# Kernel tuning notes

Measured on AMD Instinct MI355X. Metric: run time of the kernel, lower is better.

Reference implementation:

```python
import jax, jax.numpy as jnp
import numpy as np

B, T, D = 4, 2048, 768
H = 12
HD = D // H
WINDOW = 128

def setup_inputs() -> dict:
    key = jax.random.key(0)
    k1, k2, k3 = jax.random.split(key, 3)
    x = jax.random.normal(k1, (B, T, D), dtype=jnp.float32)
    Wqkv = jax.random.normal(k2, (D, 3 * D), dtype=jnp.float32) * 0.02
    Wout = jax.random.normal(k3, (D, D), dtype=jnp.float32) * 0.02
    return {"x": x, "Wqkv": Wqkv, "Wout": Wout}

def reference(x, Wqkv, Wout):
    Bx, Tx, Dx = x.shape
    qkv = x @ Wqkv                      # [B,T,3D]
    q, k, v = jnp.split(qkv, 3, axis=-1)
    def heads(t):
        return t.reshape(Bx, Tx, H, HD).transpose(0, 2, 1, 3)  # [B,H,T,hd]
    q, k, v = heads(q), heads(k), heads(v)
    scale = 1.0 / jnp.sqrt(jnp.float32(HD))
    scores = jnp.einsum('bhqd,bhkd->bhqk', q, k) * scale       # [B,H,T,T]
    pos = jnp.arange(Tx)
    dist = pos[None, :] - pos[:, None]                          # j - i
    blocked = (dist > 0) | (dist < -WINDOW)                     # causal band
    scores = jnp.where(blocked[None, None], -jnp.inf, scores)
    attn = jax.nn.softmax(scores, axis=-1)
    out = jnp.einsum('bhqk,bhkd->bhqd', attn, v)                # [B,H,T,hd]
    out = out.transpose(0, 2, 1, 3).reshape(Bx, Tx, Dx)
    return out @ Wout
```

## Files before the change

kernel.cpp:

```cpp
#include <hip/hip_runtime.h>
#include <hip/hip_bf16.h>
#include <stdint.h>

typedef unsigned short u16;
typedef __attribute__((ext_vector_type(8))) short short8;
typedef __attribute__((ext_vector_type(8))) __bf16 bf16x8;
typedef __attribute__((ext_vector_type(4))) float f32x4;

constexpr int Bc  = 4;
constexpr int Tc  = 2048;
constexpr int Dc  = 768;
constexpr int Hc  = 12;
constexpr int WINc = 128;

static __device__ __forceinline__ u16 f2bf(float f) {
  union { float f; uint32_t u; } v; v.f = f;
  uint32_t u = v.u;
  return (u16)((u + 0x7fffu + ((u >> 16) & 1u)) >> 16);
}

static __device__ __forceinline__ f32x4 mfma16x16x32(bf16x8 a, bf16x8 b, f32x4 c) {
  return __builtin_amdgcn_mfma_f32_16x16x32_bf16(a, b, c, 0, 0, 0);
}

#define GLOAD_LDS16(gsrc, ldst)                                                \
  __builtin_amdgcn_global_load_lds(                                            \
      (const __attribute__((address_space(1))) void*)(gsrc),                   \
      (__attribute__((address_space(3))) void*)(ldst), 16, 0, 0)

__global__ __launch_bounds__(256) void prep(const float* __restrict__ x,
                                            u16* __restrict__ xb,
                                            const float* __restrict__ Wqkv,
                                            u16* __restrict__ wqkvT,
                                            const float* __restrict__ Wout,
                                            u16* __restrict__ woutT) {
  __shared__ float tile[64][65];
  const int t = threadIdx.x;
  const int b = blockIdx.x;
  if (b < 6144) {
    const int i = b * 256 + t;
    const float4 f = ((const float4*)x)[i];
    union { u16 h[4]; uint2 u; } pk;
    pk.h[0] = f2bf(f.x); pk.h[1] = f2bf(f.y); pk.h[2] = f2bf(f.z); pk.h[3] = f2bf(f.w);
    ((uint2*)xb)[i] = pk.u;
    return;
  }
  const float* W; u16* WT; int C, bx, by;
  if (b < 6576) { W = Wqkv; WT = wqkvT; C = 2304; const int bb = b - 6144; bx = bb % 36; by = bb / 36; }
  else          { W = Wout; WT = woutT; C = 768;  const int bb = b - 6576; bx = bb % 12; by = bb / 12; }
  const int R = 768;
  const int c0 = bx * 64, r0 = by * 64;
#pragma unroll
  for (int i = 0; i < 16; ++i) {
    const int e = i * 256 + t;
    const int r = e >> 6, c = e & 63;
    tile[r][c] = W[(size_t)(r0 + r) * C + c0 + c];
  }
  __syncthreads();
#pragma unroll
  for (int i = 0; i < 16; ++i) {
    const int e = i * 256 + t;
    const int r = e >> 6, c = e & 63;
    WT[(size_t)(c0 + r) * R + r0 + c] = f2bf(tile[c][r]);
  }
}

template <int EPI>
__global__ __launch_bounds__(256) void gemm_bt(const u16* __restrict__ A,
                                               const u16* __restrict__ Bt,
                                               u16* __restrict__ q_ws,
                                               u16* __restrict__ k_ws,
                                               u16* __restrict__ v_ws,
                                               float* __restrict__ fout) {
  __shared__ u16 As[128][64];
  __shared__ u16 Bs[128][64];
  const int t  = threadIdx.x;
  const int w  = t >> 6, l = t & 63;
  const int lr = l & 15, lh = l >> 4;
  const int wm = w >> 1, wn = w & 1;
  const int m0 = blockIdx.y * 128, n0 = blockIdx.x * 128;

  f32x4 acc[4][4];
#pragma unroll
  for (int mi = 0; mi < 4; ++mi)
#pragma unroll
    for (int ni = 0; ni < 4; ++ni) acc[mi][ni] = f32x4{0.f, 0.f, 0.f, 0.f};

  const int srow = w * 8 + (l >> 3);
  const int scol = ((l & 7) ^ (l >> 3)) * 8;
  const u16* aP = A  + (size_t)(m0 + srow) * 768 + scol;
  const u16* bP = Bt + (size_t)(n0 + srow) * 768 + scol;
  char* asB = (char*)As + w * 1024;
  char* bsB = (char*)Bs + w * 1024;

  for (int kt = 0; kt < 12; ++kt) {
    const int ko = kt * 64;
    __syncthreads();
#pragma unroll
    for (int j = 0; j < 4; ++j) {
      GLOAD_LDS16(aP + ko + j * (32 * 768), asB + j * 4096);
      GLOAD_LDS16(bP + ko + j * (32 * 768), bsB + j * 4096);
    }
    __syncthreads();

#pragma unroll
    for (int kk = 0; kk < 2; ++kk) {
      const int cb = (kk * 64 + lh * 16) ^ ((lr & 7) << 4);
      bf16x8 af[4], bfr[4];
#pragma unroll
      for (int mi = 0; mi < 4; ++mi)
        af[mi] = *(const bf16x8*)((const char*)As + (wm * 64 + mi * 16 + lr) * 128 + cb);
#pragma unroll
      for (int ni = 0; ni < 4; ++ni)
        bfr[ni] = *(const bf16x8*)((const char*)Bs + (wn * 64 + ni * 16 + lr) * 128 + cb);
#pragma unroll
      for (int mi = 0; mi < 4; ++mi)
#pragma unroll
        for (int ni = 0; ni < 4; ++ni)
          acc[mi][ni] = mfma16x16x32(af[mi], bfr[ni], acc[mi][ni]);
    }
  }

  if (EPI == 0) {
#pragma unroll
    for (int mi = 0; mi < 4; ++mi)
#pragma unroll
      for (int ni = 0; ni < 4; ++ni) {
        const int col   = n0 + wn * 64 + ni * 16 + lr;
        const int which = col / 768;
        const int rem   = col - which * 768;
        const int h     = rem >> 6, d = rem & 63;
        u16* dst = (which == 0) ? q_ws : ((which == 1) ? k_ws : v_ws);
        const float scl = (which == 0) ? 0.125f : 1.0f;
#pragma unroll
        for (int r = 0; r < 4; ++r) {
          const int m  = m0 + wm * 64 + mi * 16 + lh * 4 + r;
          const int bb = m >> 11, tt = m & 2047;
          dst[(((size_t)(bb * Hc + h) * Tc + tt) << 6) + d] = f2bf(acc[mi][ni][r] * scl);
        }
      }
  } else {
#pragma unroll
    for (int mi = 0; mi < 4; ++mi)
#pragma unroll
      for (int ni = 0; ni < 4; ++ni) {
        const int col = n0 + wn * 64 + ni * 16 + lr;
#pragma unroll
        for (int r = 0; r < 4; ++r) {
          const int m = m0 + wm * 64 + mi * 16 + lh * 4 + r;
          fout[(size_t)m * 768 + col] = acc[mi][ni][r];
        }
      }
  }
}

__global__ __launch_bounds__(256) void swa_attn(const u16* __restrict__ Q,
                                                const u16* __restrict__ Kk,
                                                const u16* __restrict__ V,
                                                u16* __restrict__ Out) {
  __shared__ u16 Ks[3][64][72];
  __shared__ u16 Vt[3][64][72];
  __shared__ u16 Ps[4][16][72];

  const int t  = threadIdx.x;
  const int w  = t >> 6, l = t & 63;
  const int lr = l & 15, lh = l >> 4;
  const int bh = blockIdx.y;
  const int q0 = blockIdx.x * 64;
  const size_t hb = (size_t)bh * Tc * 64;

  const int kb_lo = (q0 >= WINc) ? q0 - WINc : 0;
  const int nt    = ((q0 - kb_lo) >> 6) + 1;

  const u16* qrow = Q + hb + (size_t)(q0 + w * 16 + lr) * 64;
  const bf16x8 qa0 = *(const bf16x8*)(qrow + lh * 8);
  const bf16x8 qa1 = *(const bf16x8*)(qrow + 32 + lh * 8);

  const int row = t >> 2, c = (t & 3) * 16;
  short8 kreg[3][2], vreg[3][2];
#pragma unroll
  for (int ti = 0; ti < 3; ++ti) {
    if (ti < nt) {
      const int kb = kb_lo + ti * 64;
      const short8* ksrc = (const short8*)(Kk + hb + (size_t)(kb + row) * 64 + c);
      const short8* vsrc = (const short8*)(V  + hb + (size_t)(kb + row) * 64 + c);
      kreg[ti][0] = ksrc[0]; kreg[ti][1] = ksrc[1];
      vreg[ti][0] = vsrc[0]; vreg[ti][1] = vsrc[1];
    }
  }
#pragma unroll
  for (int ti = 0; ti < 3; ++ti) {
    if (ti < nt) {
      *(short8*)&Ks[ti][row][c]     = kreg[ti][0];
      *(short8*)&Ks[ti][row][c + 8] = kreg[ti][1];
#pragma unroll
      for (int j = 0; j < 8; ++j) {
        Vt[ti][c + j][row]     = (u16)vreg[ti][0][j];
        Vt[ti][c + 8 + j][row] = (u16)vreg[ti][1][j];
      }
    }
  }
  __syncthreads();

  const short8 ones_i = {(short)0x3F80, (short)0x3F80, (short)0x3F80, (short)0x3F80,
                         (short)0x3F80, (short)0x3F80, (short)0x3F80, (short)0x3F80};
  const bf16x8 onesv = *(const bf16x8*)&ones_i;

  float m_r[4];
  f32x4 lacc = f32x4{0.f, 0.f, 0.f, 0.f};
  f32x4 Oa[4];
#pragma unroll
  for (int r = 0; r < 4; ++r) m_r[r] = -1e30f;
#pragma unroll
  for (int n = 0; n < 4; ++n) Oa[n] = f32x4{0.f, 0.f, 0.f, 0.f};

#pragma unroll
  for (int ti = 0; ti < 3; ++ti) {
    if (ti >= nt) break;
    const int kb = kb_lo + ti * 64;

    f32x4 s[4];
#pragma unroll
    for (int sub = 0; sub < 4; ++sub) {
      const bf16x8 kb0 = *(const bf16x8*)&Ks[ti][sub * 16 + lr][lh * 8];
      const bf16x8 kb1 = *(const bf16x8*)&Ks[ti][sub * 16 + lr][32 + lh * 8];
      f32x4 z = f32x4{0.f, 0.f, 0.f, 0.f};
      z = mfma16x16x32(qa0, kb0, z);
      z = mfma16x16x32(qa1, kb1, z);
      s[sub] = z;
    }

    const int qbase = q0 + w * 16 + lh * 4;
#pragma unroll
    for (int sub = 0; sub < 4; ++sub) {
      const int kj = kb + sub * 16 + lr;
#pragma unroll
      for (int r = 0; r < 4; ++r) {
        const int qi = qbase + r;
        const bool ok = (kj <= qi) && (kj + WINc >= qi);
        s[sub][r] = ok ? s[sub][r] : -1e30f;
      }
    }

    float mt[4];
#pragma unroll
    for (int r = 0; r < 4; ++r)
      mt[r] = fmaxf(fmaxf(s[0][r], s[1][r]), fmaxf(s[2][r], s[3][r]));
#pragma unroll
    for (int msk = 1; msk < 16; msk <<= 1)
#pragma unroll
      for (int r = 0; r < 4; ++r)
        mt[r] = fmaxf(mt[r], __shfl_xor(mt[r], msk, 64));

    float al[4];
#pragma unroll
    for (int r = 0; r < 4; ++r) {
      const float mn = fmaxf(m_r[r], mt[r]);
      al[r] = __expf(m_r[r] - mn);
      m_r[r] = mn;
    }

#pragma unroll
    for (int sub = 0; sub < 4; ++sub)
#pragma unroll
      for (int r = 0; r < 4; ++r)
        s[sub][r] = __expf(s[sub][r] - m_r[r]);

#pragma unroll
    for (int n = 0; n < 4; ++n)
#pragma unroll
      for (int r = 0; r < 4; ++r) Oa[n][r] *= al[r];
#pragma unroll
    for (int r = 0; r < 4; ++r) lacc[r] *= al[r];

#pragma unroll
    for (int sub = 0; sub < 4; ++sub)
#pragma unroll
      for (int r = 0; r < 4; ++r)
        Ps[w][lh * 4 + r][sub * 16 + lr] = f2bf(s[sub][r]);

#pragma unroll
    for (int ks = 0; ks < 2; ++ks) {
      const bf16x8 pa = *(const bf16x8*)&Ps[w][lr][ks * 32 + lh * 8];
      lacc = mfma16x16x32(pa, onesv, lacc);
#pragma unroll
      for (int n = 0; n < 4; ++n) {
        const bf16x8 vb = *(const bf16x8*)&Vt[ti][n * 16 + lr][ks * 32 + lh * 8];
        Oa[n] = mfma16x16x32(pa, vb, Oa[n]);
      }
    }
  }

  const int bb = bh / Hc, h = bh - bb * Hc;
#pragma unroll
  for (int r = 0; r < 4; ++r) {
    const float inv = 1.f / lacc[r];
    const int ti = q0 + w * 16 + lh * 4 + r;
#pragma unroll
    for (int n = 0; n < 4; ++n)
      Out[((size_t)(bb * Tc + ti)) * 768 + h * 64 + n * 16 + lr] =
          f2bf(Oa[n][r] * inv);
  }
}

extern "C" void kernel_launch(void* const* d_in, const int* in_sizes, int n_in,
                              void* d_out, int out_size, void* d_ws, size_t ws_size,
                              hipStream_t stream) {
  (void)in_sizes; (void)n_in; (void)out_size; (void)ws_size;
  const float* x    = (const float*)d_in[0];
  const float* Wqkv = (const float*)d_in[1];
  const float* Wout = (const float*)d_in[2];
  float* out = (float*)d_out;

  u16* ws    = (u16*)d_ws;
  u16* xb    = ws;
  u16* wqkvT = xb + 6291456;
  u16* woutT = wqkvT + 1769472;
  u16* qws   = woutT + 589824;
  u16* kws   = qws + 6291456;
  u16* vws   = kws + 6291456;
  u16* aws   = xb;

  prep<<<6720, 256, 0, stream>>>(x, xb, Wqkv, wqkvT, Wout, woutT);
  gemm_bt<0><<<dim3(18, 64), 256, 0, stream>>>(xb, wqkvT, qws, kws, vws, nullptr);
  swa_attn<<<dim3(32, 48), 256, 0, stream>>>(qws, kws, vws, aws);
  gemm_bt<1><<<dim3(6, 64), 256, 0, stream>>>(aws, woutT, nullptr, nullptr, nullptr, out);
}
```

Baseline: 106.1 us.

## Double-buffer GEMM LDS tiles to overlap global loads with MFMA compute

Makes the As/Bs shared-memory tiles double-buffered and issues the direct-to-LDS loads for the next k-tile before computing on the current one. Partial vmcnt waits plus raw s_barrier calls are meant to hide global-load latency behind the MFMA work. In exchange, LDS use per block doubles, which may lower occupancy. Correctness now depends on the hand-placed waitcnt and barrier ordering.

New measurement: 103.6 us. 1.02x faster.

```diff
diff --git a/kernel.cpp b/kernel.cpp
--- a/kernel.cpp
+++ b/kernel.cpp
@@ -72,8 +72,8 @@
                                                u16* __restrict__ k_ws,
                                                u16* __restrict__ v_ws,
                                                float* __restrict__ fout) {
-  __shared__ u16 As[128][64];
-  __shared__ u16 Bs[128][64];
+  __shared__ u16 As[2][128][64];
+  __shared__ u16 Bs[2][128][64];
   const int t  = threadIdx.x;
   const int w  = t >> 6, l = t & 63;
   const int lr = l & 15, lh = l >> 4;
@@ -90,36 +90,58 @@
   const int scol = ((l & 7) ^ (l >> 3)) * 8;
   const u16* aP = A  + (size_t)(m0 + srow) * 768 + scol;
   const u16* bP = Bt + (size_t)(n0 + srow) * 768 + scol;
-  char* asB = (char*)As + w * 1024;
-  char* bsB = (char*)Bs + w * 1024;
-
-  for (int kt = 0; kt < 12; ++kt) {
-    const int ko = kt * 64;
-    __syncthreads();
-#pragma unroll
-    for (int j = 0; j < 4; ++j) {
-      GLOAD_LDS16(aP + ko + j * (32 * 768), asB + j * 4096);
-      GLOAD_LDS16(bP + ko + j * (32 * 768), bsB + j * 4096);
-    }
-    __syncthreads();
-
-#pragma unroll
-    for (int kk = 0; kk < 2; ++kk) {
-      const int cb = (kk * 64 + lh * 16) ^ ((lr & 7) << 4);
-      bf16x8 af[4], bfr[4];
-#pragma unroll
-      for (int mi = 0; mi < 4; ++mi)
-        af[mi] = *(const bf16x8*)((const char*)As + (wm * 64 + mi * 16 + lr) * 128 + cb);
-#pragma unroll
-      for (int ni = 0; ni < 4; ++ni)
-        bfr[ni] = *(const bf16x8*)((const char*)Bs + (wn * 64 + ni * 16 + lr) * 128 + cb);
-#pragma unroll
-      for (int mi = 0; mi < 4; ++mi)
-#pragma unroll
-        for (int ni = 0; ni < 4; ++ni)
-          acc[mi][ni] = mfma16x16x32(af[mi], bfr[ni], acc[mi][ni]);
-    }
-  }
+
+#define STAGE(kt, b)                                                           \
+  {                                                                            \
+    const int ko_ = (kt) * 64;                                                 \
+    char* asB_ = (char*)As + (b) * 16384 + w * 1024;                           \
+    char* bsB_ = (char*)Bs + (b) * 16384 + w * 1024;                           \
+    _Pragma("unroll")                                                          \
+    for (int j = 0; j < 4; ++j) {                                              \
+      GLOAD_LDS16(aP + ko_ + j * (32 * 768), asB_ + j * 4096);                 \
+      GLOAD_LDS16(bP + ko_ + j * (32 * 768), bsB_ + j * 4096);                 \
+    }                                                                          \
+  }
+
+#define COMPUTE(b)                                                             \
+  {                                                                            \
+    _Pragma("unroll")                                                          \
+    for (int kk = 0; kk < 2; ++kk) {                                           \
+      const int cb = (kk * 64 + lh * 16) ^ ((lr & 7) << 4);                    \
+      bf16x8 af[4], bfr[4];                                                    \
+      _Pragma("unroll")                                                        \
+      for (int mi = 0; mi < 4; ++mi)                                           \
+        af[mi] = *(const bf16x8*)((const char*)As + (b) * 16384 +              \
+                                  (wm * 64 + mi * 16 + lr) * 128 + cb);        \
+      _Pragma("unroll")                                                        \
+      for (int ni = 0; ni < 4; ++ni)                                           \
+        bfr[ni] = *(const bf16x8*)((const char*)Bs + (b) * 16384 +             \
+                                   (wn * 64 + ni * 16 + lr) * 128 + cb);       \
+      _Pragma("unroll")                                                        \
+      for (int mi = 0; mi < 4; ++mi)                                           \
+        _Pragma("unroll")                                                      \
+        for (int ni = 0; ni < 4; ++ni)                                         \
+          acc[mi][ni] = mfma16x16x32(af[mi], bfr[ni], acc[mi][ni]);            \
+    }                                                                          \
+  }
+
+  STAGE(0, 0);
+  for (int kt = 0; kt < 11; ++kt) {
+    const int b = kt & 1;
+    STAGE(kt + 1, b ^ 1);
+    asm volatile("s_waitcnt vmcnt(8)" ::: "memory");
+    __builtin_amdgcn_sched_barrier(0);
+    __builtin_amdgcn_s_barrier();
+    COMPUTE(b);
+    __builtin_amdgcn_s_barrier();
+  }
+  asm volatile("s_waitcnt vmcnt(0)" ::: "memory");
+  __builtin_amdgcn_sched_barrier(0);
+  __builtin_amdgcn_s_barrier();
+  COMPUTE(1);
+
+#undef STAGE
+#undef COMPUTE
 
   if (EPI == 0) {
 #pragma unroll
```
